# Kernel optimization log

Hardware: AMD Instinct MI355X
Metric: run time of the kernel (lower is better)

Reference implementation:

```python
import jax, jax.numpy as jnp
import numpy as np

N, F, H, C = 50000, 128, 4, 32  # nodes, in-features, heads, per-head dim
E = 800000
D = H * C  # concat output dim = 128


def _tconv(x, src, dst, ea, Wq, bq, Wk, bk, Wv, bv, We, Ws, bs):
    # PyG TransformerConv (concat=True, root_weight=True, beta=False, eval mode)
    n = x.shape[0]
    q = (x @ Wq + bq).reshape(n, H, C)
    k = (x @ Wk + bk).reshape(n, H, C)
    v = (x @ Wv + bv).reshape(n, H, C)
    e = (ea @ We).reshape(-1, H, C)            # edge embedding [E,H,C]
    kj = k[src] + e                            # gathered keys + edge emb
    alpha = jnp.einsum('ehc,ehc->eh', q[dst], kj) / jnp.sqrt(jnp.float32(C))
    amax = jax.ops.segment_max(alpha, dst, num_segments=n)
    ex = jnp.exp(alpha - amax[dst])
    denom = jax.ops.segment_sum(ex, dst, num_segments=n)
    w = ex / (denom[dst] + 1e-16)              # segment softmax over in-edges
    msg = (v[src] + e) * w[:, :, None]
    out = jax.ops.segment_sum(msg, dst, num_segments=n).reshape(n, D)
    return out + x @ Ws + bs                   # skip connection


def setup_inputs() -> dict:
    key = jax.random.key(0)
    ks = jax.random.split(key, 24)
    s = lambda i, shape, scale: jax.random.normal(ks[i], shape, dtype=jnp.float32) * scale
    inp = {
        'x': s(0, (N, F), 1.0),
        'edge_index': jax.random.randint(ks[1], (2, E), 0, N),
        'edge_attr': s(2, (E,), 1.0),
        # layer 1 (in = F)
        'Wq1': s(3, (F, D), 1.0 / np.sqrt(F)), 'bq1': jnp.zeros((D,), jnp.float32),
        'Wk1': s(4, (F, D), 1.0 / np.sqrt(F)), 'bk1': jnp.zeros((D,), jnp.float32),
        'Wv1': s(5, (F, D), 1.0 / np.sqrt(F)), 'bv1': jnp.zeros((D,), jnp.float32),
        'We1': s(6, (1, D), 1.0),
        'Ws1': s(7, (F, D), 1.0 / np.sqrt(F)), 'bs1': jnp.zeros((D,), jnp.float32),
        # layer 2 (in = D)
        'Wq2': s(8, (D, D), 1.0 / np.sqrt(D)), 'bq2': jnp.zeros((D,), jnp.float32),
        'Wk2': s(9, (D, D), 1.0 / np.sqrt(D)), 'bk2': jnp.zeros((D,), jnp.float32),
        'Wv2': s(10, (D, D), 1.0 / np.sqrt(D)), 'bv2': jnp.zeros((D,), jnp.float32),
        'We2': s(11, (1, D), 1.0),
        'Ws2': s(12, (D, D), 1.0 / np.sqrt(D)), 'bs2': jnp.zeros((D,), jnp.float32),
    }
    return inp


def reference(x, edge_index, edge_attr,
              Wq1, bq1, Wk1, bk1, Wv1, bv1, We1, Ws1, bs1,
              Wq2, bq2, Wk2, bk2, Wv2, bv2, We2, Ws2, bs2):
    src, dst = edge_index[0], edge_index[1]
    ea = edge_attr.reshape(-1, 1)
    h = _tconv(x, src, dst, ea, Wq1, bq1, Wk1, bk1, Wv1, bv1, We1, Ws1, bs1)
    h = jax.nn.relu(h)  # dropout is identity in eval mode
    h = _tconv(h, src, dst, ea, Wq2, bq2, Wk2, bk2, Wv2, bv2, We2, Ws2, bs2)
    return jax.nn.relu(h)
```

## Files before the change

### kernel.cpp

```cpp
#include <hip/hip_runtime.h>


#define TPB 256

typedef __attribute__((ext_vector_type(8))) short short8v;
typedef __attribute__((ext_vector_type(4))) float f32x4;

__device__ __forceinline__ unsigned short f2bf(float f) {
    unsigned u = __float_as_uint(f);
    u = (u + 0x7FFFu + ((u >> 16) & 1u)) >> 16;
    return (unsigned short)u;
}
__device__ __forceinline__ float bf2f(unsigned short s) {
    return __uint_as_float((unsigned)s << 16);
}
__device__ __forceinline__ float4 bf4_to_f4(ushort4 u) {
    return make_float4(bf2f(u.x), bf2f(u.y), bf2f(u.z), bf2f(u.w));
}
__device__ __forceinline__ float exp2_hw(float x) {
    float r;
    asm("v_exp_f32 %0, %1" : "=v"(r) : "v"(x));
    return r;
}

__global__ void __launch_bounds__(TPB) prepack_k(
    const float* __restrict__ Wq1, const float* __restrict__ Wk1,
    const float* __restrict__ Wv1, const float* __restrict__ Ws1,
    const float* __restrict__ Wq2, const float* __restrict__ Wk2,
    const float* __restrict__ Wv2, const float* __restrict__ Ws2,
    unsigned short* __restrict__ pack)
{
    int i = blockIdx.x * TPB + threadIdx.x;
    int j = i & 7, l = (i >> 3) & 63, t = (i >> 9) & 3, c = (i >> 11) & 7, g = (i >> 14) & 7;
    const float* Wt[8] = {Wq1, Wk1, Wv1, Ws1, Wq2, Wk2, Wv2, Ws2};
    const float* W = Wt[g];
    int kk = t * 32 + (l >> 4) * 8 + j;
    int nn = c * 16 + (l & 15);
    pack[i] = f2bf(W[kk * 128 + nn]);
}

template <bool AF32>
__global__ void __launch_bounds__(TPB) gemm_mfma_k(
    const void* __restrict__ Av, int M,
    const unsigned short* __restrict__ pack,
    const float* __restrict__ bq, const float* __restrict__ bk,
    const float* __restrict__ bv, const float* __restrict__ bs,
    unsigned short* __restrict__ oq, unsigned short* __restrict__ ok,
    unsigned short* __restrict__ ov, float* __restrict__ os)
{
    const int g = blockIdx.y;
    const int row0 = blockIdx.x * 128;
    const int wv = threadIdx.x >> 6;
    const int lane = threadIdx.x & 63;
    const int rbase = row0 + wv * 32;
    const int rlo = lane & 15;
    const int kg = (lane >> 4) * 8;
    const int rof = (lane >> 4) * 4;

    const short8v z8 = {0, 0, 0, 0, 0, 0, 0, 0};
    short8v a[2][4];
#pragma unroll
    for (int m = 0; m < 2; ++m) {
        int row = rbase + m * 16 + rlo;
        if (row >= M) {
#pragma unroll
            for (int t = 0; t < 4; ++t) a[m][t] = z8;
        } else if (AF32) {
            const float* Af = (const float*)Av + (size_t)row * 128 + kg;
#pragma unroll
            for (int t = 0; t < 4; ++t) {
                float4 lo = *(const float4*)(Af + t * 32);
                float4 hi = *(const float4*)(Af + t * 32 + 4);
                short8v p;
                p[0] = (short)f2bf(lo.x); p[1] = (short)f2bf(lo.y);
                p[2] = (short)f2bf(lo.z); p[3] = (short)f2bf(lo.w);
                p[4] = (short)f2bf(hi.x); p[5] = (short)f2bf(hi.y);
                p[6] = (short)f2bf(hi.z); p[7] = (short)f2bf(hi.w);
                a[m][t] = p;
            }
        } else {
            const unsigned short* Ab = (const unsigned short*)Av + (size_t)row * 128 + kg;
#pragma unroll
            for (int t = 0; t < 4; ++t)
                a[m][t] = *(const short8v*)(Ab + t * 32);
        }
    }

    f32x4 acc[2][8];
#pragma unroll
    for (int m = 0; m < 2; ++m)
#pragma unroll
        for (int c = 0; c < 8; ++c)
            acc[m][c] = (f32x4){0.f, 0.f, 0.f, 0.f};

    const unsigned short* bp = pack + (size_t)g * (8 * 4 * 512);
#pragma unroll
    for (int c = 0; c < 8; ++c) {
        short8v b[4];
#pragma unroll
        for (int t = 0; t < 4; ++t)
            b[t] = *(const short8v*)(bp + (c * 4 + t) * 512 + lane * 8);
#pragma unroll
        for (int t = 0; t < 4; ++t) {
            acc[0][c] = __builtin_amdgcn_mfma_f32_16x16x32_bf16(a[0][t], b[t], acc[0][c], 0, 0, 0);
            acc[1][c] = __builtin_amdgcn_mfma_f32_16x16x32_bf16(a[1][t], b[t], acc[1][c], 0, 0, 0);
        }
    }

    const float* bias = g == 0 ? bq : (g == 1 ? bk : (g == 2 ? bv : bs));
    if (g == 3) {
#pragma unroll
        for (int c = 0; c < 8; ++c) {
            float bb = bias[c * 16 + rlo];
#pragma unroll
            for (int m = 0; m < 2; ++m)
#pragma unroll
                for (int j = 0; j < 4; ++j) {
                    int row = rbase + m * 16 + rof + j;
                    if (row < M) os[(size_t)row * 128 + c * 16 + rlo] = acc[m][c][j] + bb;
                }
        }
    } else {
        unsigned short* out = g == 0 ? oq : (g == 1 ? ok : ov);
#pragma unroll
        for (int c = 0; c < 8; ++c) {
            float bb = bias[c * 16 + rlo];
#pragma unroll
            for (int m = 0; m < 2; ++m)
#pragma unroll
                for (int j = 0; j < 4; ++j) {
                    int row = rbase + m * 16 + rof + j;
                    if (row < M) out[(size_t)row * 128 + c * 16 + rlo] = f2bf(acc[m][c][j] + bb);
                }
        }
    }
}

__global__ void __launch_bounds__(TPB) hist_k(const int* __restrict__ dst,
                                              int* __restrict__ deg, int E)
{
    int e = blockIdx.x * TPB + threadIdx.x;
    if (e < E) atomicAdd(&deg[dst[e]], 1);
}

__global__ void __launch_bounds__(TPB) scan_a_k(const int* __restrict__ deg, int n,
                                                int* __restrict__ incl,
                                                int* __restrict__ bsum)
{
    __shared__ int ts[TPB];
    const int base = blockIdx.x * 1024;
    int vals[4], s = 0;
#pragma unroll
    for (int j = 0; j < 4; ++j) {
        int i = base + threadIdx.x * 4 + j;
        vals[j] = (i < n) ? deg[i] : 0;
        s += vals[j];
    }
    ts[threadIdx.x] = s;
    __syncthreads();
    for (int off = 1; off < TPB; off <<= 1) {
        int u = (threadIdx.x >= off) ? ts[threadIdx.x - off] : 0;
        __syncthreads();
        ts[threadIdx.x] += u;
        __syncthreads();
    }
    int run = ts[threadIdx.x] - s;
#pragma unroll
    for (int j = 0; j < 4; ++j) {
        run += vals[j];
        int i = base + threadIdx.x * 4 + j;
        if (i < n) incl[i] = run;
    }
    if (threadIdx.x == TPB - 1) bsum[blockIdx.x] = ts[TPB - 1];
}

__global__ void __launch_bounds__(TPB) scan_b_k(int* __restrict__ bsum, int nb)
{
    __shared__ int ts[TPB];
    int t = threadIdx.x;
    int v = (t < nb) ? bsum[t] : 0;
    ts[t] = v;
    __syncthreads();
    for (int off = 1; off < TPB; off <<= 1) {
        int u = (t >= off) ? ts[t - off] : 0;
        __syncthreads();
        ts[t] += u;
        __syncthreads();
    }
    if (t < nb) bsum[t] = ts[t] - v;
}

__global__ void __launch_bounds__(TPB) finalize_k(const int* __restrict__ incl,
                                                  const int* __restrict__ deg,
                                                  const int* __restrict__ bsum, int n,
                                                  int* __restrict__ row_ptr,
                                                  int* __restrict__ cursor)
{
    const int base = blockIdx.x * 1024;
    const int boff = bsum[blockIdx.x];
#pragma unroll
    for (int j = 0; j < 4; ++j) {
        int i = base + threadIdx.x * 4 + j;
        if (i < n) {
            int iv = incl[i] + boff;
            int st = iv - deg[i];
            row_ptr[i] = st;
            cursor[i] = st;
            if (i == n - 1) row_ptr[n] = iv;
        }
    }
}

__global__ void __launch_bounds__(TPB) scatter_k(
    const int* __restrict__ src, const int* __restrict__ dst,
    const float* __restrict__ ea, int* __restrict__ cursor,
    int2* __restrict__ csr_pair, int E)
{
    int e = blockIdx.x * TPB + threadIdx.x;
    if (e >= E) return;
    int pos = atomicAdd(&cursor[dst[e]], 1);
    csr_pair[pos] = make_int2(src[e], __float_as_int(ea[e]));
}

template <bool BF16OUT>
__global__ void __launch_bounds__(TPB) node_attn_k(
    const unsigned short* __restrict__ q, const unsigned short* __restrict__ k,
    const unsigned short* __restrict__ v, const float* __restrict__ skip,
    const float* __restrict__ We,
    const int* __restrict__ row_ptr, const int2* __restrict__ csr_pair,
    void* __restrict__ outp, int n)
{
    const int node = blockIdx.x * 8 + (threadIdx.x >> 5);
    if (node >= n) return;
    const int l32 = threadIdx.x & 31;
    const int c4 = l32 * 4;

    const float C2 = 0.17677669529663687f * 1.44269504088896f;
    const float4 we4 = *(const float4*)(We + c4);
    float4 qv = bf4_to_f4(*(const ushort4*)(q + (size_t)node * 128 + c4));
    qv.x *= C2; qv.y *= C2; qv.z *= C2; qv.w *= C2;

    float qwe = qv.x * we4.x + qv.y * we4.y + qv.z * we4.z + qv.w * we4.w;
    qwe += __shfl_xor(qwe, 1);
    qwe += __shfl_xor(qwe, 2);
    qwe += __shfl_xor(qwe, 4);

    const int p0 = row_ptr[node], p1 = row_ptr[node + 1];

    float m = -3.4e38f, l = 0.f, sae = 0.f;
    float4 acc = make_float4(0.f, 0.f, 0.f, 0.f);

    int j = p0;
    for (; j + 4 <= p1; j += 4) {
        int2 pr0 = csr_pair[j],     pr1 = csr_pair[j + 1];
        int2 pr2 = csr_pair[j + 2], pr3 = csr_pair[j + 3];
        ushort4 ku0 = *(const ushort4*)(k + (unsigned)pr0.x * 128u + c4);
        ushort4 ku1 = *(const ushort4*)(k + (unsigned)pr1.x * 128u + c4);
        ushort4 ku2 = *(const ushort4*)(k + (unsigned)pr2.x * 128u + c4);
        ushort4 ku3 = *(const ushort4*)(k + (unsigned)pr3.x * 128u + c4);
        ushort4 vu0 = *(const ushort4*)(v + (unsigned)pr0.x * 128u + c4);
        ushort4 vu1 = *(const ushort4*)(v + (unsigned)pr1.x * 128u + c4);
        ushort4 vu2 = *(const ushort4*)(v + (unsigned)pr2.x * 128u + c4);
        ushort4 vu3 = *(const ushort4*)(v + (unsigned)pr3.x * 128u + c4);
        float4 kf0 = bf4_to_f4(ku0), kf1 = bf4_to_f4(ku1);
        float4 kf2 = bf4_to_f4(ku2), kf3 = bf4_to_f4(ku3);
        float d0 = kf0.x * qv.x + kf0.y * qv.y + kf0.z * qv.z + kf0.w * qv.w;
        float d1 = kf1.x * qv.x + kf1.y * qv.y + kf1.z * qv.z + kf1.w * qv.w;
        float d2 = kf2.x * qv.x + kf2.y * qv.y + kf2.z * qv.z + kf2.w * qv.w;
        float d3 = kf3.x * qv.x + kf3.y * qv.y + kf3.z * qv.z + kf3.w * qv.w;
        d0 += __shfl_xor(d0, 1); d0 += __shfl_xor(d0, 2); d0 += __shfl_xor(d0, 4);
        d1 += __shfl_xor(d1, 1); d1 += __shfl_xor(d1, 2); d1 += __shfl_xor(d1, 4);
        d2 += __shfl_xor(d2, 1); d2 += __shfl_xor(d2, 2); d2 += __shfl_xor(d2, 4);
        d3 += __shfl_xor(d3, 1); d3 += __shfl_xor(d3, 2); d3 += __shfl_xor(d3, 4);
        float al0 = fmaf(__int_as_float(pr0.y), qwe, d0);
        float al1 = fmaf(__int_as_float(pr1.y), qwe, d1);
        float al2 = fmaf(__int_as_float(pr2.y), qwe, d2);
        float al3 = fmaf(__int_as_float(pr3.y), qwe, d3);
        float mn = fmaxf(m, fmaxf(fmaxf(al0, al1), fmaxf(al2, al3)));
        float sc = exp2_hw(m - mn);
        float pe0 = exp2_hw(al0 - mn), pe1 = exp2_hw(al1 - mn);
        float pe2 = exp2_hw(al2 - mn), pe3 = exp2_hw(al3 - mn);
        float4 vf0 = bf4_to_f4(vu0), vf1 = bf4_to_f4(vu1);
        float4 vf2 = bf4_to_f4(vu2), vf3 = bf4_to_f4(vu3);
        l = fmaf(l, sc, (pe0 + pe1) + (pe2 + pe3));
        sae = fmaf(sae, sc, fmaf(pe3, __int_as_float(pr3.y),
                   fmaf(pe2, __int_as_float(pr2.y),
                   fmaf(pe1, __int_as_float(pr1.y), pe0 * __int_as_float(pr0.y)))));
        acc.x = fmaf(acc.x, sc, fmaf(pe0, vf0.x, fmaf(pe1, vf1.x, fmaf(pe2, vf2.x, pe3 * vf3.x))));
        acc.y = fmaf(acc.y, sc, fmaf(pe0, vf0.y, fmaf(pe1, vf1.y, fmaf(pe2, vf2.y, pe3 * vf3.y))));
        acc.z = fmaf(acc.z, sc, fmaf(pe0, vf0.z, fmaf(pe1, vf1.z, fmaf(pe2, vf2.z, pe3 * vf3.z))));
        acc.w = fmaf(acc.w, sc, fmaf(pe0, vf0.w, fmaf(pe1, vf1.w, fmaf(pe2, vf2.w, pe3 * vf3.w))));
        m = mn;
    }
    for (; j < p1; ++j) {
        int2 pr0 = csr_pair[j];
        ushort4 ku0 = *(const ushort4*)(k + (unsigned)pr0.x * 128u + c4);
        ushort4 vu0 = *(const ushort4*)(v + (unsigned)pr0.x * 128u + c4);
        float4 kf0 = bf4_to_f4(ku0);
        float d0 = kf0.x * qv.x + kf0.y * qv.y + kf0.z * qv.z + kf0.w * qv.w;
        d0 += __shfl_xor(d0, 1); d0 += __shfl_xor(d0, 2); d0 += __shfl_xor(d0, 4);
        float al0 = fmaf(__int_as_float(pr0.y), qwe, d0);
        float mn = fmaxf(m, al0);
        float sc = exp2_hw(m - mn);
        float pe0 = exp2_hw(al0 - mn);
        float4 vf0 = bf4_to_f4(vu0);
        l = fmaf(l, sc, pe0);
        sae = fmaf(sae, sc, pe0 * __int_as_float(pr0.y));
        acc.x = fmaf(acc.x, sc, pe0 * vf0.x);
        acc.y = fmaf(acc.y, sc, pe0 * vf0.y);
        acc.z = fmaf(acc.z, sc, pe0 * vf0.z);
        acc.w = fmaf(acc.w, sc, pe0 * vf0.w);
        m = mn;
    }

    float inv = 1.f / (l + 1e-16f);
    float4 sk = *(const float4*)(skip + (size_t)node * 128 + c4);
    float o0 = fmaxf(fmaf(fmaf(sae, we4.x, acc.x), inv, sk.x), 0.f);
    float o1 = fmaxf(fmaf(fmaf(sae, we4.y, acc.y), inv, sk.y), 0.f);
    float o2 = fmaxf(fmaf(fmaf(sae, we4.z, acc.z), inv, sk.z), 0.f);
    float o3 = fmaxf(fmaf(fmaf(sae, we4.w, acc.w), inv, sk.w), 0.f);
    if (BF16OUT) {
        ushort4 o;
        o.x = f2bf(o0); o.y = f2bf(o1); o.z = f2bf(o2); o.w = f2bf(o3);
        *(ushort4*)((unsigned short*)outp + (size_t)node * 128 + c4) = o;
    } else {
        *(float4*)((float*)outp + (size_t)node * 128 + c4) =
            make_float4(o0, o1, o2, o3);
    }
}

extern "C" void kernel_launch(void* const* d_in, const int* in_sizes, int n_in,
                              void* d_out, int out_size, void* d_ws, size_t ws_size,
                              hipStream_t stream)
{
    const float* x   = (const float*)d_in[0];
    const int*   ei  = (const int*)d_in[1];
    const float* ea  = (const float*)d_in[2];
    const float* Wq1 = (const float*)d_in[3];  const float* bq1 = (const float*)d_in[4];
    const float* Wk1 = (const float*)d_in[5];  const float* bk1 = (const float*)d_in[6];
    const float* Wv1 = (const float*)d_in[7];  const float* bv1 = (const float*)d_in[8];
    const float* We1 = (const float*)d_in[9];
    const float* Ws1 = (const float*)d_in[10]; const float* bs1 = (const float*)d_in[11];
    const float* Wq2 = (const float*)d_in[12]; const float* bq2 = (const float*)d_in[13];
    const float* Wk2 = (const float*)d_in[14]; const float* bk2 = (const float*)d_in[15];
    const float* Wv2 = (const float*)d_in[16]; const float* bv2 = (const float*)d_in[17];
    const float* We2 = (const float*)d_in[18];
    const float* Ws2 = (const float*)d_in[19]; const float* bs2 = (const float*)d_in[20];

    const int N = in_sizes[0] / 128;
    const int E = in_sizes[1] / 2;
    const int* src = ei;
    const int* dst = ei + E;
    float* outf = (float*)d_out;

    unsigned short* q  = (unsigned short*)d_ws;
    unsigned short* k  = q + (size_t)N * 128;
    unsigned short* v  = k + (size_t)N * 128;
    float*          s  = (float*)(v + (size_t)N * 128);
    unsigned short* xb = (unsigned short*)(s + (size_t)N * 128);
    unsigned short* pk = xb + (size_t)N * 128;
    int*   row_ptr = (int*)(pk + 131072);
    int*   deg     = row_ptr + (N + 1);
    int*   incl    = deg + N;
    int*   cursor  = incl + N;
    int*   bsum    = cursor + N;
    int2*  csr_pair = (int2*)(bsum + 256 + 1);

    csr_pair = (int2*)(((uintptr_t)(bsum + 256) + 7) & ~(uintptr_t)7);

    const int gE   = (E + TPB - 1) / TPB;
    const int nb   = (N + 1023) / 1024;
    const int gN8  = (N + 7) / 8;
    const int gG   = (N + 127) / 128;
    const dim3 gGd(gG, 4);

    hipMemsetAsync(deg, 0, (size_t)N * sizeof(int), stream);
    hist_k<<<gE, TPB, 0, stream>>>(dst, deg, E);
    scan_a_k<<<nb, TPB, 0, stream>>>(deg, N, incl, bsum);
    scan_b_k<<<1, TPB, 0, stream>>>(bsum, nb);
    finalize_k<<<nb, TPB, 0, stream>>>(incl, deg, bsum, N, row_ptr, cursor);
    scatter_k<<<gE, TPB, 0, stream>>>(src, dst, ea, cursor, csr_pair, E);

    prepack_k<<<131072 / TPB, TPB, 0, stream>>>(Wq1, Wk1, Wv1, Ws1,
                                                Wq2, Wk2, Wv2, Ws2, pk);

    gemm_mfma_k<true><<<gGd, TPB, 0, stream>>>(x, N, pk, bq1, bk1, bv1, bs1,
                                               q, k, v, s);
    node_attn_k<true><<<gN8, TPB, 0, stream>>>(q, k, v, s, We1, row_ptr, csr_pair,
                                               xb, N);
    gemm_mfma_k<false><<<gGd, TPB, 0, stream>>>(xb, N, pk + 65536, bq2, bk2, bv2, bs2,
                                                q, k, v, s);
    node_attn_k<false><<<gN8, TPB, 0, stream>>>(q, k, v, s, We2, row_ptr, csr_pair,
                                                outf, N);
}
```

Measured before the change: 315.9 us.

## Use 16 lanes per node with 8-wide bf16 loads in attention kernel

Each node is now handled by 16 lanes, each processing 8 channels with 16-byte loads, instead of 32 lanes processing 4 channels. This halves the shuffle reductions per edge, widens the gathers, and packs 16 nodes per block. The scalar remainder loop is replaced by clamped indices and masked logits inside the 4-wide loop, which removes divergent tail code but issues redundant gathers for partial groups. Register pressure per lane rises with the 8-element arrays.

```diff
diff --git a/kernel.cpp b/kernel.cpp
--- a/kernel.cpp
+++ b/kernel.cpp
@@ -4,6 +4,7 @@
 #define TPB 256
 
 typedef __attribute__((ext_vector_type(8))) short short8v;
+typedef __attribute__((ext_vector_type(8))) unsigned short ushort8v;
 typedef __attribute__((ext_vector_type(4))) float f32x4;
 
 __device__ __forceinline__ unsigned short f2bf(float f) {
@@ -13,9 +14,6 @@
 }
 __device__ __forceinline__ float bf2f(unsigned short s) {
     return __uint_as_float((unsigned)s << 16);
-}
-__device__ __forceinline__ float4 bf4_to_f4(ushort4 u) {
-    return make_float4(bf2f(u.x), bf2f(u.y), bf2f(u.z), bf2f(u.w));
 }
 __device__ __forceinline__ float exp2_hw(float x) {
     float r;
@@ -230,102 +228,108 @@
     const int* __restrict__ row_ptr, const int2* __restrict__ csr_pair,
     void* __restrict__ outp, int n)
 {
-    const int node = blockIdx.x * 8 + (threadIdx.x >> 5);
+    const int node = blockIdx.x * 16 + (threadIdx.x >> 4);
     if (node >= n) return;
-    const int l32 = threadIdx.x & 31;
-    const int c4 = l32 * 4;
+    const int l16 = threadIdx.x & 15;
+    const int c8 = l16 * 8;
 
     const float C2 = 0.17677669529663687f * 1.44269504088896f;
-    const float4 we4 = *(const float4*)(We + c4);
-    float4 qv = bf4_to_f4(*(const ushort4*)(q + (size_t)node * 128 + c4));
-    qv.x *= C2; qv.y *= C2; qv.z *= C2; qv.w *= C2;
-
-    float qwe = qv.x * we4.x + qv.y * we4.y + qv.z * we4.z + qv.w * we4.w;
+
+    float we8[8], qv[8];
+    {
+        float4 wlo = *(const float4*)(We + c8);
+        float4 whi = *(const float4*)(We + c8 + 4);
+        we8[0] = wlo.x; we8[1] = wlo.y; we8[2] = wlo.z; we8[3] = wlo.w;
+        we8[4] = whi.x; we8[5] = whi.y; we8[6] = whi.z; we8[7] = whi.w;
+        ushort8v qu = *(const ushort8v*)(q + (size_t)node * 128 + c8);
+#pragma unroll
+        for (int i = 0; i < 8; ++i) qv[i] = bf2f((unsigned short)qu[i]) * C2;
+    }
+
+    float qwe = 0.f;
+#pragma unroll
+    for (int i = 0; i < 8; ++i) qwe = fmaf(qv[i], we8[i], qwe);
     qwe += __shfl_xor(qwe, 1);
     qwe += __shfl_xor(qwe, 2);
-    qwe += __shfl_xor(qwe, 4);
 
     const int p0 = row_ptr[node], p1 = row_ptr[node + 1];
 
     float m = -3.4e38f, l = 0.f, sae = 0.f;
-    float4 acc = make_float4(0.f, 0.f, 0.f, 0.f);
-
-    int j = p0;
-    for (; j + 4 <= p1; j += 4) {
-        int2 pr0 = csr_pair[j],     pr1 = csr_pair[j + 1];
-        int2 pr2 = csr_pair[j + 2], pr3 = csr_pair[j + 3];
-        ushort4 ku0 = *(const ushort4*)(k + (unsigned)pr0.x * 128u + c4);
-        ushort4 ku1 = *(const ushort4*)(k + (unsigned)pr1.x * 128u + c4);
-        ushort4 ku2 = *(const ushort4*)(k + (unsigned)pr2.x * 128u + c4);
-        ushort4 ku3 = *(const ushort4*)(k + (unsigned)pr3.x * 128u + c4);
-        ushort4 vu0 = *(const ushort4*)(v + (unsigned)pr0.x * 128u + c4);
-        ushort4 vu1 = *(const ushort4*)(v + (unsigned)pr1.x * 128u + c4);
-        ushort4 vu2 = *(const ushort4*)(v + (unsigned)pr2.x * 128u + c4);
-        ushort4 vu3 = *(const ushort4*)(v + (unsigned)pr3.x * 128u + c4);
-        float4 kf0 = bf4_to_f4(ku0), kf1 = bf4_to_f4(ku1);
-        float4 kf2 = bf4_to_f4(ku2), kf3 = bf4_to_f4(ku3);
-        float d0 = kf0.x * qv.x + kf0.y * qv.y + kf0.z * qv.z + kf0.w * qv.w;
-        float d1 = kf1.x * qv.x + kf1.y * qv.y + kf1.z * qv.z + kf1.w * qv.w;
-        float d2 = kf2.x * qv.x + kf2.y * qv.y + kf2.z * qv.z + kf2.w * qv.w;
-        float d3 = kf3.x * qv.x + kf3.y * qv.y + kf3.z * qv.z + kf3.w * qv.w;
-        d0 += __shfl_xor(d0, 1); d0 += __shfl_xor(d0, 2); d0 += __shfl_xor(d0, 4);
-        d1 += __shfl_xor(d1, 1); d1 += __shfl_xor(d1, 2); d1 += __shfl_xor(d1, 4);
-        d2 += __shfl_xor(d2, 1); d2 += __shfl_xor(d2, 2); d2 += __shfl_xor(d2, 4);
-        d3 += __shfl_xor(d3, 1); d3 += __shfl_xor(d3, 2); d3 += __shfl_xor(d3, 4);
-        float al0 = fmaf(__int_as_float(pr0.y), qwe, d0);
-        float al1 = fmaf(__int_as_float(pr1.y), qwe, d1);
-        float al2 = fmaf(__int_as_float(pr2.y), qwe, d2);
-        float al3 = fmaf(__int_as_float(pr3.y), qwe, d3);
+    float acc[8];
+#pragma unroll
+    for (int i = 0; i < 8; ++i) acc[i] = 0.f;
+
+    for (int j = p0; j < p1; j += 4) {
+        const int last = p1 - 1;
+        int2 pr0 = csr_pair[j];
+        int2 pr1 = csr_pair[min(j + 1, last)];
+        int2 pr2 = csr_pair[min(j + 2, last)];
+        int2 pr3 = csr_pair[min(j + 3, last)];
+        ushort8v ku0 = *(const ushort8v*)(k + (unsigned)pr0.x * 128u + c8);
+        ushort8v ku1 = *(const ushort8v*)(k + (unsigned)pr1.x * 128u + c8);
+        ushort8v ku2 = *(const ushort8v*)(k + (unsigned)pr2.x * 128u + c8);
+        ushort8v ku3 = *(const ushort8v*)(k + (unsigned)pr3.x * 128u + c8);
+        ushort8v vu0 = *(const ushort8v*)(v + (unsigned)pr0.x * 128u + c8);
+        ushort8v vu1 = *(const ushort8v*)(v + (unsigned)pr1.x * 128u + c8);
+        ushort8v vu2 = *(const ushort8v*)(v + (unsigned)pr2.x * 128u + c8);
+        ushort8v vu3 = *(const ushort8v*)(v + (unsigned)pr3.x * 128u + c8);
+
+        float d0 = 0.f, d1 = 0.f, d2 = 0.f, d3 = 0.f;
+#pragma unroll
+        for (int i = 0; i < 8; ++i) {
+            d0 = fmaf(bf2f((unsigned short)ku0[i]), qv[i], d0);
+            d1 = fmaf(bf2f((unsigned short)ku1[i]), qv[i], d1);
+            d2 = fmaf(bf2f((unsigned short)ku2[i]), qv[i], d2);
+            d3 = fmaf(bf2f((unsigned short)ku3[i]), qv[i], d3);
+        }
+        d0 += __shfl_xor(d0, 1); d0 += __shfl_xor(d0, 2);
+        d1 += __shfl_xor(d1, 1); d1 += __shfl_xor(d1, 2);
+        d2 += __shfl_xor(d2, 1); d2 += __shfl_xor(d2, 2);
+        d3 += __shfl_xor(d3, 1); d3 += __shfl_xor(d3, 2);
+
+        float ea0 = __int_as_float(pr0.y), ea1 = __int_as_float(pr1.y);
+        float ea2 = __int_as_float(pr2.y), ea3 = __int_as_float(pr3.y);
+        float al0 = fmaf(ea0, qwe, d0);
+        float al1 = (j + 1 < p1) ? fmaf(ea1, qwe, d1) : -3.4e38f;
+        float al2 = (j + 2 < p1) ? fmaf(ea2, qwe, d2) : -3.4e38f;
+        float al3 = (j + 3 < p1) ? fmaf(ea3, qwe, d3) : -3.4e38f;
+
         float mn = fmaxf(m, fmaxf(fmaxf(al0, al1), fmaxf(al2, al3)));
         float sc = exp2_hw(m - mn);
         float pe0 = exp2_hw(al0 - mn), pe1 = exp2_hw(al1 - mn);
         float pe2 = exp2_hw(al2 - mn), pe3 = exp2_hw(al3 - mn);
-        float4 vf0 = bf4_to_f4(vu0), vf1 = bf4_to_f4(vu1);
-        float4 vf2 = bf4_to_f4(vu2), vf3 = bf4_to_f4(vu3);
+
         l = fmaf(l, sc, (pe0 + pe1) + (pe2 + pe3));
-        sae = fmaf(sae, sc, fmaf(pe3, __int_as_float(pr3.y),
-                   fmaf(pe2, __int_as_float(pr2.y),
-                   fmaf(pe1, __int_as_float(pr1.y), pe0 * __int_as_float(pr0.y)))));
-        acc.x = fmaf(acc.x, sc, fmaf(pe0, vf0.x, fmaf(pe1, vf1.x, fmaf(pe2, vf2.x, pe3 * vf3.x))));
-        acc.y = fmaf(acc.y, sc, fmaf(pe0, vf0.y, fmaf(pe1, vf1.y, fmaf(pe2, vf2.y, pe3 * vf3.y))));
-        acc.z = fmaf(acc.z, sc, fmaf(pe0, vf0.z, fmaf(pe1, vf1.z, fmaf(pe2, vf2.z, pe3 * vf3.z))));
-        acc.w = fmaf(acc.w, sc, fmaf(pe0, vf0.w, fmaf(pe1, vf1.w, fmaf(pe2, vf2.w, pe3 * vf3.w))));
+        sae = fmaf(sae, sc, fmaf(pe3, ea3, fmaf(pe2, ea2, fmaf(pe1, ea1, pe0 * ea0))));
+#pragma unroll
+        for (int i = 0; i < 8; ++i) {
+            float mv = fmaf(pe0, bf2f((unsigned short)vu0[i]),
+                       fmaf(pe1, bf2f((unsigned short)vu1[i]),
+                       fmaf(pe2, bf2f((unsigned short)vu2[i]),
+                            pe3 * bf2f((unsigned short)vu3[i]))));
+            acc[i] = fmaf(acc[i], sc, mv);
+        }
         m = mn;
     }
-    for (; j < p1; ++j) {
-        int2 pr0 = csr_pair[j];
-        ushort4 ku0 = *(const ushort4*)(k + (unsigned)pr0.x * 128u + c4);
-        ushort4 vu0 = *(const ushort4*)(v + (unsigned)pr0.x * 128u + c4);
-        float4 kf0 = bf4_to_f4(ku0);
-        float d0 = kf0.x * qv.x + kf0.y * qv.y + kf0.z * qv.z + kf0.w * qv.w;
-        d0 += __shfl_xor(d0, 1); d0 += __shfl_xor(d0, 2); d0 += __shfl_xor(d0, 4);
-        float al0 = fmaf(__int_as_float(pr0.y), qwe, d0);
-        float mn = fmaxf(m, al0);
-        float sc = exp2_hw(m - mn);
-        float pe0 = exp2_hw(al0 - mn);
-        float4 vf0 = bf4_to_f4(vu0);
-        l = fmaf(l, sc, pe0);
-        sae = fmaf(sae, sc, pe0 * __int_as_float(pr0.y));
-        acc.x = fmaf(acc.x, sc, pe0 * vf0.x);
-        acc.y = fmaf(acc.y, sc, pe0 * vf0.y);
-        acc.z = fmaf(acc.z, sc, pe0 * vf0.z);
-        acc.w = fmaf(acc.w, sc, pe0 * vf0.w);
-        m = mn;
-    }
 
     float inv = 1.f / (l + 1e-16f);
-    float4 sk = *(const float4*)(skip + (size_t)node * 128 + c4);
-    float o0 = fmaxf(fmaf(fmaf(sae, we4.x, acc.x), inv, sk.x), 0.f);
-    float o1 = fmaxf(fmaf(fmaf(sae, we4.y, acc.y), inv, sk.y), 0.f);
-    float o2 = fmaxf(fmaf(fmaf(sae, we4.z, acc.z), inv, sk.z), 0.f);
-    float o3 = fmaxf(fmaf(fmaf(sae, we4.w, acc.w), inv, sk.w), 0.f);
+    float4 sklo = *(const float4*)(skip + (size_t)node * 128 + c8);
+    float4 skhi = *(const float4*)(skip + (size_t)node * 128 + c8 + 4);
+    float sk[8] = {sklo.x, sklo.y, sklo.z, sklo.w, skhi.x, skhi.y, skhi.z, skhi.w};
+    float o[8];
+#pragma unroll
+    for (int i = 0; i < 8; ++i)
+        o[i] = fmaxf(fmaf(fmaf(sae, we8[i], acc[i]), inv, sk[i]), 0.f);
+
     if (BF16OUT) {
-        ushort4 o;
-        o.x = f2bf(o0); o.y = f2bf(o1); o.z = f2bf(o2); o.w = f2bf(o3);
-        *(ushort4*)((unsigned short*)outp + (size_t)node * 128 + c4) = o;
+        ushort8v ov;
+#pragma unroll
+        for (int i = 0; i < 8; ++i) ov[i] = f2bf(o[i]);
+        *(ushort8v*)((unsigned short*)outp + (size_t)node * 128 + c8) = ov;
     } else {
-        *(float4*)((float*)outp + (size_t)node * 128 + c4) =
-            make_float4(o0, o1, o2, o3);
+        float* op = (float*)outp + (size_t)node * 128 + c8;
+        *(float4*)op = make_float4(o[0], o[1], o[2], o[3]);
+        *(float4*)(op + 4) = make_float4(o[4], o[5], o[6], o[7]);
     }
 }
 
@@ -364,13 +368,11 @@
     int*   incl    = deg + N;
     int*   cursor  = incl + N;
     int*   bsum    = cursor + N;
-    int2*  csr_pair = (int2*)(bsum + 256 + 1);
-
-    csr_pair = (int2*)(((uintptr_t)(bsum + 256) + 7) & ~(uintptr_t)7);
+    int2*  csr_pair = (int2*)(((uintptr_t)(bsum + 256) + 7) & ~(uintptr_t)7);
 
     const int gE   = (E + TPB - 1) / TPB;
     const int nb   = (N + 1023) / 1024;
-    const int gN8  = (N + 7) / 8;
+    const int gN16 = (N + 15) / 16;
     const int gG   = (N + 127) / 128;
     const dim3 gGd(gG, 4);
 
@@ -386,10 +388,10 @@
 
     gemm_mfma_k<true><<<gGd, TPB, 0, stream>>>(x, N, pk, bq1, bk1, bv1, bs1,
                                                q, k, v, s);
-    node_attn_k<true><<<gN8, TPB, 0, stream>>>(q, k, v, s, We1, row_ptr, csr_pair,
-                                               xb, N);
+    node_attn_k<true><<<gN16, TPB, 0, stream>>>(q, k, v, s, We1, row_ptr, csr_pair,
+                                                xb, N);
     gemm_mfma_k<false><<<gGd, TPB, 0, stream>>>(xb, N, pk + 65536, bq2, bk2, bv2, bs2,
                                                 q, k, v, s);
-    node_attn_k<false><<<gN8, TPB, 0, stream>>>(q, k, v, s, We2, row_ptr, csr_pair,
-                                                outf, N);
-}
+    node_attn_k<false><<<gN16, TPB, 0, stream>>>(q, k, v, s, We2, row_ptr, csr_pair,
+                                                 outf, N);
+}
```

Result: no change. 312.8 us (-1.0%).
